# Kernel tuning notes

Hardware: AMD Instinct MI355X
Metric: run time of the kernel (lower is better)

The kernel has to match this reference:

```python
import jax, jax.numpy as jnp
import numpy as np
import math

EMBED_DIM = 1024
N_HEAD = 16
HEAD_DIM = EMBED_DIM // N_HEAD


def setup_inputs() -> dict:
    key = jax.random.key(0)
    ks = jax.random.split(key, 9)
    B, T, C = 4, 2048, EMBED_DIM
    s = 1.0 / math.sqrt(C)
    return {
        "x": jax.random.normal(ks[0], (B, T, C), dtype=jnp.float32),
        "Wq": jax.random.normal(ks[1], (C, C), dtype=jnp.float32) * s,
        "bq": jnp.zeros((C,), dtype=jnp.float32),
        "Wk": jax.random.normal(ks[2], (C, C), dtype=jnp.float32) * s,
        "bk": jnp.zeros((C,), dtype=jnp.float32),
        "Wv": jax.random.normal(ks[3], (C, C), dtype=jnp.float32) * s,
        "bv": jnp.zeros((C,), dtype=jnp.float32),
        "Wp": jax.random.normal(ks[4], (C, C), dtype=jnp.float32) * s,
        "bp": jnp.zeros((C,), dtype=jnp.float32),
    }


def reference(x, Wq, bq, Wk, bk, Wv, bv, Wp, bp):
    B, T, C = x.shape
    H, D = N_HEAD, HEAD_DIM

    def heads(W, b):
        # [B,T,C] -> [B,H,T,D]
        return (x @ W.T + b).reshape(B, T, H, D).transpose(0, 2, 1, 3)

    q = heads(Wq, bq)
    k = heads(Wk, bk)
    v = heads(Wv, bv)

    att = jnp.einsum("bhtd,bhsd->bhts", q, k) * (1.0 / math.sqrt(D))
    causal = jnp.tril(jnp.ones((T, T), dtype=bool))
    att = jnp.where(causal[None, None], att, -jnp.inf)
    att = jax.nn.softmax(att, axis=-1)
    y = jnp.einsum("bhts,bhsd->bhtd", att, v)  # [B,H,T,D]
    y = y.transpose(0, 2, 1, 3).reshape(B, T, C)
    return y @ Wp.T + bp
```

## Files before the change

kernel.cpp:

```cpp
#include <hip/hip_runtime.h>
#include <hip/hip_bf16.h>
#include <cstdint>
#include <cstddef>

#define TQ 2048
#define CDIM 1024
#define NH 16
#define HD 64

typedef __attribute__((ext_vector_type(8))) short bf16x8;
typedef __attribute__((ext_vector_type(4))) float f32x4;
typedef __attribute__((ext_vector_type(16))) float f32x16;

__device__ __forceinline__ unsigned short f2bf(float f) {
  union { float f; unsigned u; } x; x.f = f;
  unsigned r = x.u + 0x7fffu + ((x.u >> 16) & 1u);
  return (unsigned short)(r >> 16);
}

__device__ __forceinline__ unsigned cvtpk(float lo, float hi) {
  unsigned r;
  asm("v_cvt_pk_bf16_f32 %0, %1, %2" : "=v"(r) : "v"(lo), "v"(hi));
  return r;
}

__device__ __forceinline__ void plswap(unsigned& x, unsigned& y) {
  asm("v_permlane32_swap_b32 %0, %1" : "+v"(x), "+v"(y));
}

__device__ __forceinline__ float exp2_fast(float x) {
  float r;
  asm("v_exp_f32 %0, %1" : "=v"(r) : "v"(x));
  return r;
}

__device__ __forceinline__ void gload_lds16(const void* g, void* l) {
  typedef __attribute__((address_space(1))) const void gv;
  typedef __attribute__((address_space(3))) void lv;
  __builtin_amdgcn_global_load_lds((gv*)g, (lv*)l, 16, 0, 0);
}

#define BAR() do { asm volatile("" ::: "memory"); __builtin_amdgcn_s_barrier(); asm volatile("" ::: "memory"); } while (0)
#define VMC2() asm volatile("s_waitcnt vmcnt(2)" ::: "memory")
#define VMC0() asm volatile("s_waitcnt vmcnt(0)" ::: "memory")

__global__ void cvt_all_kernel(const float* __restrict__ x,
                               const float* __restrict__ w0, const float* __restrict__ w1,
                               const float* __restrict__ w2, const float* __restrict__ w3,
                               unsigned short* __restrict__ xb,
                               unsigned short* __restrict__ wb) {
  const int bid = (int)blockIdx.x;
  if (bid < 4096) {
    for (int i = bid * 256 + threadIdx.x; i < 2097152; i += 4096 * 256) {
      float4 v = *(const float4*)(x + (size_t)i * 4);
      ushort4 o;
      o.x = f2bf(v.x); o.y = f2bf(v.y); o.z = f2bf(v.z); o.w = f2bf(v.w);
      *(ushort4*)(xb + (size_t)i * 4) = o;
    }
  } else {
    int i = (bid - 4096) * 256 + threadIdx.x;
    int which = i >> 18;
    const float* src = which == 0 ? w0 : which == 1 ? w1 : which == 2 ? w2 : w3;
    int off = (i & 262143) * 4;
    float4 v = *(const float4*)(src + off);
    ushort4 o;
    o.x = f2bf(v.x); o.y = f2bf(v.y); o.z = f2bf(v.z); o.w = f2bf(v.w);
    *(ushort4*)(wb + (size_t)i * 4) = o;
  }
}

template <int EPI>
__global__ __launch_bounds__(512, 2) void gemm256_kernel(
    const unsigned short* __restrict__ A,
    const unsigned short* __restrict__ Bt,
    const float* __restrict__ b0, const float* __restrict__ b1,
    void* __restrict__ outp,
    int M, int N, int K) {
  __shared__ __align__(16) char lds[131072];

  const int tid = (int)threadIdx.x;
  const int w = tid >> 6, lane = tid & 63;
  const int g = lane >> 4, c = lane & 15;
  const int wm = w >> 2, wn = w & 3;

  const int nbm = M >> 8, nbn = N >> 8;
  const int nwg = nbm * nbn;
  int id = (int)blockIdx.x;
  const int cpx = nwg >> 3;
  id = (id & 7) * cpx + (id >> 3);
  const int tn = id % nbn, tm = id / nbn;

  const char* Ab = (const char*)(A + (size_t)tm * 256 * K);
  const char* Bb = (const char*)(Bt + (size_t)tn * 256 * K);
  const int rowB = K * 2;
  const int nht = (K >> 6) << 2;

  char* aw = lds + wm * 16384;
  char* bw = lds + 65536 + (wn >> 1) * 16384;
  const int bfo = (wn & 1) * 8;

  auto stage_ht = [&](int j) {
    if (j >= nht) return;
    const int t = j >> 2, part = j & 3;
    const int isB = part >> 1, half = part & 1;
    const char* src = isB ? Bb : Ab;
    char* dst = lds + isB * 65536 + (t & 1) * 32768 + half * 16384 + w * 2048;
#pragma unroll
    for (int r = 0; r < 2; ++r) {
      const int f = w * 2 + r;
      const int m16 = f >> 1, ki = f & 1;
      gload_lds16(src + (size_t)(half * 128 + m16 * 16 + c) * rowB +
                      t * 128 + ki * 64 + g * 16,
                  dst + r * 1024);
    }
  };

  f32x4 acc[8][4];
#pragma unroll
  for (int i = 0; i < 8; ++i)
#pragma unroll
    for (int j = 0; j < 4; ++j) acc[i][j] = (f32x4){0.f, 0.f, 0.f, 0.f};
  bf16x8 af[4][2], bv[2][2];

  auto rdA = [&](int buf, int ms) {
#pragma unroll
    for (int mi = 0; mi < 4; ++mi)
#pragma unroll
      for (int ki = 0; ki < 2; ++ki)
        af[mi][ki] = *(const bf16x8*)(aw + buf * 32768 +
                                      ((ms * 4 + mi) * 2 + ki) * 1024 + lane * 16);
  };
  auto rdB = [&](int buf, int ns) {
#pragma unroll
    for (int ni = 0; ni < 2; ++ni)
#pragma unroll
      for (int ki = 0; ki < 2; ++ki)
        bv[ni][ki] = *(const bf16x8*)(bw + buf * 32768 +
                                      (bfo + (ns * 2 + ni) * 2 + ki) * 1024 + lane * 16);
  };
  auto mm = [&](int ms, int ns) {
    __builtin_amdgcn_s_setprio(1);
#pragma unroll
    for (int mi = 0; mi < 4; ++mi)
#pragma unroll
      for (int ni = 0; ni < 2; ++ni)
#pragma unroll
        for (int ki = 0; ki < 2; ++ki)
          acc[ms * 4 + mi][ns * 2 + ni] = __builtin_amdgcn_mfma_f32_16x16x32_bf16(
              af[mi][ki], bv[ni][ki], acc[ms * 4 + mi][ns * 2 + ni], 0, 0, 0);
    __builtin_amdgcn_s_setprio(0);
  };

  for (int j = 0; j < 5; ++j) stage_ht(j);
  VMC2();
  BAR();

  const int niter = K >> 7;
#pragma unroll 1
  for (int i = 0; i < niter; ++i) {
    const int j0 = 5 + (i << 3);
    rdA(0, 0); rdB(0, 0); stage_ht(j0 + 0); BAR(); mm(0, 0); BAR();
    rdB(0, 1);            stage_ht(j0 + 1); BAR(); mm(0, 1); BAR();
    rdA(0, 1);            stage_ht(j0 + 2); BAR(); mm(1, 1); BAR();
    rdB(0, 0);            stage_ht(j0 + 3);
    if (i + 1 < niter) { VMC2(); } else { VMC0(); }
    BAR(); mm(1, 0); BAR();
    rdA(1, 0); rdB(1, 0); stage_ht(j0 + 4); BAR(); mm(0, 0); BAR();
    rdB(1, 1);            stage_ht(j0 + 5); BAR(); mm(0, 1); BAR();
    rdA(1, 1);            stage_ht(j0 + 6); BAR(); mm(1, 1); BAR();
    rdB(1, 0);            stage_ht(j0 + 7); VMC2(); BAR(); mm(1, 0); BAR();
  }

#pragma unroll
  for (int mi = 0; mi < 8; ++mi) {
#pragma unroll
    for (int ni = 0; ni < 4; ++ni) {
      const int n = tn * 256 + wn * 64 + ni * 16 + c;
#pragma unroll
      for (int e = 0; e < 4; ++e) {
        const int m = tm * 256 + wm * 128 + mi * 16 + g * 4 + e;
        float v = acc[mi][ni][e];
        if (EPI == 4) {
          unsigned short* O = (unsigned short*)outp;
          if (n < 1024) {
            v = (v + b0[n]) * 0.18033688f;
            size_t idx = ((size_t)(m >> 11) * NH + (n >> 6)) * (TQ * HD) +
                         (size_t)(m & (TQ - 1)) * HD + (n & (HD - 1));
            O[idx] = f2bf(v);
          } else {
            int nn = n - 1024;
            v += b1[nn];
            size_t idx = 8388608 + ((size_t)(m >> 11) * NH + (nn >> 6)) * (TQ * HD) +
                         (size_t)(m & (TQ - 1)) * HD + (nn & (HD - 1));
            O[idx] = f2bf(v);
          }
        }
      }
    }
  }
}

template <int EPI, int ROWMAJ>
__global__ __launch_bounds__(512, 2) void gemm128x256_kernel(
    const unsigned short* __restrict__ A,
    const unsigned short* __restrict__ Bt,
    const float* __restrict__ b0, const float* __restrict__ b1,
    void* __restrict__ outp,
    int M, int N, int K) {
  __shared__ __align__(16) char lds[98304];

  const int tid = (int)threadIdx.x;
  const int w = tid >> 6, lane = tid & 63;
  const int g = lane >> 4, c = lane & 15;
  const int wm = w >> 2, wn = w & 3;

  const int nbm = M >> 7, nbn = N >> 8;
  const int nwg = nbm * nbn;
  int id = (int)blockIdx.x;
  const int cpx = nwg >> 3;
  id = (id & 7) * cpx + (id >> 3);
  const int tm = ROWMAJ ? (id / nbn) : (id % nbm);
  const int tn = ROWMAJ ? (id % nbn) : (id / nbm);

  const char* Ab = (const char*)(A + (size_t)tm * 128 * K);
  const char* Bb = (const char*)(Bt + (size_t)tn * 256 * K);
  const int rowB = K * 2;
  const int nt = K >> 6;

  auto stageA = [&](int t) {
    if (t >= nt) return;
    char* dst = lds + (t & 1) * 49152 + (w << 11);
    const char* s = Ab + (size_t)(w * 16 + c) * rowB + t * 128 + g * 16;
    gload_lds16(s, dst);
    gload_lds16(s + 64, dst + 1024);
  };
  auto stageB = [&](int t, int odd) {
    if (t >= nt) return;
    const int n16 = (w >> 1) * 4 + 2 * odd + (w & 1);
    char* dst = lds + (t & 1) * 49152 + 16384 + (n16 << 11);
    const char* s = Bb + (size_t)(n16 * 16 + c) * rowB + t * 128 + g * 16;
    gload_lds16(s, dst);
    gload_lds16(s + 64, dst + 1024);
  };

  f32x4 acc[4][4];
#pragma unroll
  for (int i = 0; i < 4; ++i)
#pragma unroll
    for (int j = 0; j < 4; ++j) acc[i][j] = (f32x4){0.f, 0.f, 0.f, 0.f};
  bf16x8 af[2][2], bv[2][2][2];

  auto rdA = [&](int cur, int ms) {
#pragma unroll
    for (int mi2 = 0; mi2 < 2; ++mi2)
#pragma unroll
      for (int ki = 0; ki < 2; ++ki)
        af[mi2][ki] = *(const bf16x8*)(lds + cur * 49152 +
            (((wm * 4 + ms * 2 + mi2) << 1) + ki) * 1024 + lane * 16);
  };
  auto rdB = [&](int cur, int ns) {
#pragma unroll
    for (int ni2 = 0; ni2 < 2; ++ni2)
#pragma unroll
      for (int ki = 0; ki < 2; ++ki)
        bv[ns][ni2][ki] = *(const bf16x8*)(lds + cur * 49152 + 16384 +
            (((wn * 4 + ns * 2 + ni2) << 1) + ki) * 1024 + lane * 16);
  };
  auto mm = [&](int ms, int ns) {
    __builtin_amdgcn_s_setprio(1);
#pragma unroll
    for (int mi2 = 0; mi2 < 2; ++mi2)
#pragma unroll
      for (int ni2 = 0; ni2 < 2; ++ni2)
#pragma unroll
        for (int ki = 0; ki < 2; ++ki)
          acc[ms * 2 + mi2][ns * 2 + ni2] = __builtin_amdgcn_mfma_f32_16x16x32_bf16(
              af[mi2][ki], bv[ns][ni2][ki], acc[ms * 2 + mi2][ns * 2 + ni2], 0, 0, 0);
    __builtin_amdgcn_s_setprio(0);
  };

  stageA(0); stageB(0, 0); stageB(0, 1);
  VMC2();
  BAR();

#pragma unroll 1
  for (int i = 0; i < (nt >> 1); ++i) {
    const int t0 = 2 * i, t1 = 2 * i + 1;
    rdA(0, 0); rdB(0, 0); stageA(t0 + 1);
    mm(0, 0); VMC2(); BAR();
    rdB(0, 1); stageB(t0 + 1, 0);
    mm(0, 1); BAR();
    rdA(0, 1); stageB(t0 + 1, 1);
    mm(1, 1); BAR();
    mm(1, 0); VMC2(); BAR();
    rdA(1, 0); rdB(1, 0); stageA(t1 + 1);
    mm(0, 0);
    if (t1 == nt - 1) { VMC0(); } else { VMC2(); }
    BAR();
    rdB(1, 1); stageB(t1 + 1, 0);
    mm(0, 1); BAR();
    rdA(1, 1); stageB(t1 + 1, 1);
    mm(1, 1); BAR();
    mm(1, 0); VMC2(); BAR();
  }

#pragma unroll
  for (int mi = 0; mi < 4; ++mi) {
#pragma unroll
    for (int ni = 0; ni < 4; ++ni) {
      const int n = tn * 256 + wn * 64 + ni * 16 + c;
#pragma unroll
      for (int e = 0; e < 4; ++e) {
        const int m = tm * 128 + wm * 64 + mi * 16 + g * 4 + e;
        float v = acc[mi][ni][e];
        if (EPI == 1) {
          v += b0[m];
          size_t idx = ((size_t)(n >> 11) * (NH * HD) + m) * TQ + (n & (TQ - 1));
          ((unsigned short*)outp)[idx] = f2bf(v);
        } else if (EPI == 2) {
          v += b0[n];
          ((float*)outp)[(size_t)m * N + n] = v;
        }
      }
    }
  }
}

__global__ __launch_bounds__(256, 4) void attn_kernel(
    const unsigned short* __restrict__ Q,
    const unsigned short* __restrict__ K,
    const unsigned short* __restrict__ Vt,
    unsigned short* __restrict__ Y) {
  __shared__ __align__(16) char Ks[2][8192];
  __shared__ __align__(16) char Vs[2][8192];

  const int tid = (int)threadIdx.x;
  const int w = tid >> 6, lane = tid & 63;
  const int l31 = lane & 31, hi = lane >> 5;

  const int n = (int)blockIdx.x;
  const int g = n & 255, k = n >> 8;
  const int bh = g >> 2;
  const int u = 2 * (g & 3) + (k >> 1);
  const int qt = (k & 1) ? (15 - u) : u;
  const int b = bh >> 4, h = bh & 15;

  const unsigned short* Qb = Q + (size_t)bh * TQ * HD;
  const char* Kb = (const char*)(K + (size_t)bh * TQ * HD);
  const char* Vb = (const char*)(Vt + (size_t)bh * HD * TQ);

  auto stage = [&](int buf, int kt) {
#pragma unroll
    for (int i = 0; i < 2; ++i) {
      const int s = i * 256 + tid;
      const int r32 = (s >> 8) * 32 + (s & 31);
      const int ck = ((s >> 6) & 3) * 32 + ((s >> 5) & 1) * 16;
      char* kdst = &Ks[buf][0] + i * 4096 + (w << 10);
      char* vdst = &Vs[buf][0] + i * 4096 + (w << 10);
      gload_lds16(Kb + (size_t)kt * 8192 + r32 * 128 + ck, kdst);
      gload_lds16(Vb + (size_t)r32 * 4096 + kt * 128 + ck, vdst);
    }
  };

  const int q0 = qt * 128 + w * 32;
  const int qg = q0 + l31;
  const int nkv = 2 * qt + 2;

  stage(0, 0);

  bf16x8 qf[4];
#pragma unroll
  for (int dk = 0; dk < 4; ++dk)
    qf[dk] = *(const bf16x8*)(Qb + (size_t)qg * HD + dk * 16 + hi * 8);

  f32x16 oac[2];
#pragma unroll
  for (int nb = 0; nb < 2; ++nb)
#pragma unroll
    for (int r = 0; r < 16; ++r) oac[nb][r] = 0.f;
  float mr = -3.0e38f, lr = 0.f;

  __syncthreads();

  for (int kt = 0; kt < nkv; ++kt) {
    const int cur = kt & 1;
    if (kt + 1 < nkv) stage(cur ^ 1, kt + 1);

    if (kt * 64 <= q0 + 31) {
      const char* Klane = &Ks[cur][0] + lane * 16;
      const char* Vlane = &Vs[cur][0] + lane * 16;

      f32x16 s0, s1;
#pragma unroll
      for (int r = 0; r < 16; ++r) { s0[r] = 0.f; s1[r] = 0.f; }
#pragma unroll
      for (int dk = 0; dk < 4; ++dk) {
        bf16x8 kf0 = *(const bf16x8*)(Klane + (dk << 10));
        bf16x8 kf1 = *(const bf16x8*)(Klane + ((4 + dk) << 10));
        s0 = __builtin_amdgcn_mfma_f32_32x32x16_bf16(kf0, qf[dk], s0, 0, 0, 0);
        s1 = __builtin_amdgcn_mfma_f32_32x32x16_bf16(kf1, qf[dk], s1, 0, 0, 0);
      }

      const bool maskT = (kt * 64 + 63 > q0);
      if (maskT) {
#pragma unroll
        for (int r = 0; r < 16; ++r) {
          int kv0 = kt * 64 + ((r & 3) + 8 * (r >> 2)) + 4 * hi;
          s0[r] = (kv0 <= qg) ? s0[r] : -3.0e38f;
          s1[r] = (kv0 + 32 <= qg) ? s1[r] : -3.0e38f;
        }
      }

      float mt_ = s0[0];
#pragma unroll
      for (int r = 1; r < 16; ++r) mt_ = fmaxf(mt_, s0[r]);
#pragma unroll
      for (int r = 0; r < 16; ++r) mt_ = fmaxf(mt_, s1[r]);
      mt_ = fmaxf(mt_, __shfl_xor(mt_, 32));

      if (!__all(mt_ - mr <= 8.0f)) {
        const float mn = fmaxf(mr, mt_);
        const float al = exp2_fast(mr - mn);
        mr = mn;
        lr *= al;
#pragma unroll
        for (int nb = 0; nb < 2; ++nb)
#pragma unroll
          for (int r = 0; r < 16; ++r) oac[nb][r] *= al;
      }

      float rs = 0.f;
#pragma unroll
      for (int r = 0; r < 16; ++r) { s0[r] = exp2_fast(s0[r] - mr); rs += s0[r]; }
#pragma unroll
      for (int r = 0; r < 16; ++r) { s1[r] = exp2_fast(s1[r] - mr); rs += s1[r]; }
      rs += __shfl_xor(rs, 32);
      lr += rs;

      bf16x8 pf[4];
      {
        unsigned a0 = cvtpk(s0[0], s0[1]), b0 = cvtpk(s0[2], s0[3]);
        unsigned c0 = cvtpk(s0[4], s0[5]), d0 = cvtpk(s0[6], s0[7]);
        plswap(a0, c0); plswap(b0, d0);
        unsigned a1 = cvtpk(s0[8], s0[9]), b1 = cvtpk(s0[10], s0[11]);
        unsigned c1 = cvtpk(s0[12], s0[13]), d1 = cvtpk(s0[14], s0[15]);
        plswap(a1, c1); plswap(b1, d1);
        unsigned a2 = cvtpk(s1[0], s1[1]), b2 = cvtpk(s1[2], s1[3]);
        unsigned c2 = cvtpk(s1[4], s1[5]), d2 = cvtpk(s1[6], s1[7]);
        plswap(a2, c2); plswap(b2, d2);
        unsigned a3 = cvtpk(s1[8], s1[9]), b3 = cvtpk(s1[10], s1[11]);
        unsigned c3 = cvtpk(s1[12], s1[13]), d3 = cvtpk(s1[14], s1[15]);
        plswap(a3, c3); plswap(b3, d3);
        union { unsigned u[4]; bf16x8 v; } t;
        t.u[0] = a0; t.u[1] = b0; t.u[2] = c0; t.u[3] = d0; pf[0] = t.v;
        t.u[0] = a1; t.u[1] = b1; t.u[2] = c1; t.u[3] = d1; pf[1] = t.v;
        t.u[0] = a2; t.u[1] = b2; t.u[2] = c2; t.u[3] = d2; pf[2] = t.v;
        t.u[0] = a3; t.u[1] = b3; t.u[2] = c3; t.u[3] = d3; pf[3] = t.v;
      }

#pragma unroll
      for (int nb = 0; nb < 2; ++nb)
#pragma unroll
        for (int ks = 0; ks < 4; ++ks) {
          bf16x8 vf = *(const bf16x8*)(Vlane + (((nb << 2) + ks) << 10));
          oac[nb] = __builtin_amdgcn_mfma_f32_32x32x16_bf16(vf, pf[ks], oac[nb], 0, 0, 0);
        }
    }
    __syncthreads();
  }

  float inv;
  asm("v_rcp_f32 %0, %1" : "=v"(inv) : "v"(lr));
  unsigned short* Yrow = Y + (size_t)(b * TQ + qg) * CDIM + h * 64;
#pragma unroll
  for (int nb = 0; nb < 2; ++nb)
#pragma unroll
    for (int j = 0; j < 8; ++j) {
      const int dbase = ((2 * j) & 3) + 8 * (j >> 1);
      unsigned lo = f2bf(oac[nb][2 * j] * inv);
      unsigned hi2 = f2bf(oac[nb][2 * j + 1] * inv);
      *(unsigned*)(Yrow + nb * 32 + dbase + 4 * hi) = lo | (hi2 << 16);
    }
}

extern "C" void kernel_launch(void* const* d_in, const int* in_sizes, int n_in,
                              void* d_out, int out_size, void* d_ws, size_t ws_size,
                              hipStream_t stream) {
  (void)in_sizes; (void)n_in; (void)out_size; (void)ws_size;
  const float* x  = (const float*)d_in[0];
  const float* Wq = (const float*)d_in[1];
  const float* bq = (const float*)d_in[2];
  const float* Wk = (const float*)d_in[3];
  const float* bk = (const float*)d_in[4];
  const float* Wv = (const float*)d_in[5];
  const float* bv = (const float*)d_in[6];
  const float* Wp = (const float*)d_in[7];
  const float* bp = (const float*)d_in[8];
  float* out = (float*)d_out;

  char* ws = (char*)d_ws;
  unsigned short* xb  = (unsigned short*)(ws + 0);
  unsigned short* wqb = (unsigned short*)(ws + 16777216);
  unsigned short* wvb = (unsigned short*)(ws + 20971520);
  unsigned short* wpb = (unsigned short*)(ws + 23068672);
  unsigned short* Qh  = (unsigned short*)(ws + 25165824);
  unsigned short* Kh  = (unsigned short*)(ws + 41943040);
  unsigned short* Vt  = (unsigned short*)(ws + 58720256);
  unsigned short* y   = (unsigned short*)(ws + 75497472);

  cvt_all_kernel<<<8192, 256, 0, stream>>>(x, Wq, Wk, Wv, Wp, xb, wqb);

  gemm256_kernel<4><<<256, 512, 0, stream>>>(xb, wqb, bq, bk, Qh, 8192, 2048, 1024);
  gemm128x256_kernel<1, 0><<<256, 512, 0, stream>>>(wvb, xb, bv, bv, Vt, 1024, 8192, 1024);

  attn_kernel<<<1024, 256, 0, stream>>>(Qh, Kh, Vt, y);

  gemm128x256_kernel<2, 1><<<256, 512, 0, stream>>>(y, wpb, bp, bp, out, 8192, 1024, 1024);
}
```

Measured before the change: 196.8 us.

## Process two heads per attention block to raise per-wave ILP

Each attention workgroup now handles the same query tile for two (batch, head) pairs, staging K/V for both into a 64KB double-buffered LDS region and interleaving their independent QK, softmax and PV chains. The grid is halved to 512 blocks and launch bounds drop to 2 blocks per CU. The intent is to expose more independent MFMA and exp work per wave to hide latency. The cost is higher register and LDS use, which lowers occupancy, and fewer blocks to balance the causal work.

```diff
diff --git a/kernel.cpp b/kernel.cpp
--- a/kernel.cpp
+++ b/kernel.cpp
@@ -326,28 +326,31 @@
   }
 }
 
-__global__ __launch_bounds__(256, 4) void attn_kernel(
+__global__ __launch_bounds__(256, 2) void attn_kernel(
     const unsigned short* __restrict__ Q,
     const unsigned short* __restrict__ K,
     const unsigned short* __restrict__ Vt,
     unsigned short* __restrict__ Y) {
-  __shared__ __align__(16) char Ks[2][8192];
-  __shared__ __align__(16) char Vs[2][8192];
+  __shared__ __align__(16) char L[2][32768];
 
   const int tid = (int)threadIdx.x;
   const int w = tid >> 6, lane = tid & 63;
   const int l31 = lane & 31, hi = lane >> 5;
 
-  const int n = (int)blockIdx.x;
-  const int g = n & 255, k = n >> 8;
-  const int bh = g >> 2;
-  const int u = 2 * (g & 3) + (k >> 1);
-  const int qt = (k & 1) ? (15 - u) : u;
-  const int b = bh >> 4, h = bh & 15;
-
-  const unsigned short* Qb = Q + (size_t)bh * TQ * HD;
-  const char* Kb = (const char*)(K + (size_t)bh * TQ * HD);
-  const char* Vb = (const char*)(Vt + (size_t)bh * HD * TQ);
+  const int z = (int)blockIdx.x;
+  const int kk = z >> 8, r_ = z & 255;
+  const int u = r_ & 7, bhp = r_ >> 3;
+  const int qt = kk ? (15 - u) : u;
+  const int bh0 = 2 * bhp, bh1 = 2 * bhp + 1;
+  const int b0i = bh0 >> 4, h0 = bh0 & 15;
+  const int b1i = bh1 >> 4, h1 = bh1 & 15;
+
+  const unsigned short* QbA = Q + (size_t)bh0 * TQ * HD;
+  const unsigned short* QbB = Q + (size_t)bh1 * TQ * HD;
+  const char* KbA = (const char*)(K + (size_t)bh0 * TQ * HD);
+  const char* KbB = (const char*)(K + (size_t)bh1 * TQ * HD);
+  const char* VbA = (const char*)(Vt + (size_t)bh0 * HD * TQ);
+  const char* VbB = (const char*)(Vt + (size_t)bh1 * HD * TQ);
 
   auto stage = [&](int buf, int kt) {
 #pragma unroll
@@ -355,10 +358,12 @@
       const int s = i * 256 + tid;
       const int r32 = (s >> 8) * 32 + (s & 31);
       const int ck = ((s >> 6) & 3) * 32 + ((s >> 5) & 1) * 16;
-      char* kdst = &Ks[buf][0] + i * 4096 + (w << 10);
-      char* vdst = &Vs[buf][0] + i * 4096 + (w << 10);
-      gload_lds16(Kb + (size_t)kt * 8192 + r32 * 128 + ck, kdst);
-      gload_lds16(Vb + (size_t)r32 * 4096 + kt * 128 + ck, vdst);
+      const int doff = i * 4096 + (w << 10);
+      char* base = &L[buf][0];
+      gload_lds16(KbA + (size_t)kt * 8192 + r32 * 128 + ck, base + doff);
+      gload_lds16(KbB + (size_t)kt * 8192 + r32 * 128 + ck, base + 8192 + doff);
+      gload_lds16(VbA + (size_t)r32 * 4096 + kt * 128 + ck, base + 16384 + doff);
+      gload_lds16(VbB + (size_t)r32 * 4096 + kt * 128 + ck, base + 24576 + doff);
     }
   };
 
@@ -368,17 +373,19 @@
 
   stage(0, 0);
 
-  bf16x8 qf[4];
-#pragma unroll
-  for (int dk = 0; dk < 4; ++dk)
-    qf[dk] = *(const bf16x8*)(Qb + (size_t)qg * HD + dk * 16 + hi * 8);
-
-  f32x16 oac[2];
+  bf16x8 qfA[4], qfB[4];
+#pragma unroll
+  for (int dk = 0; dk < 4; ++dk) {
+    qfA[dk] = *(const bf16x8*)(QbA + (size_t)qg * HD + dk * 16 + hi * 8);
+    qfB[dk] = *(const bf16x8*)(QbB + (size_t)qg * HD + dk * 16 + hi * 8);
+  }
+
+  f32x16 oacA[2], oacB[2];
 #pragma unroll
   for (int nb = 0; nb < 2; ++nb)
 #pragma unroll
-    for (int r = 0; r < 16; ++r) oac[nb][r] = 0.f;
-  float mr = -3.0e38f, lr = 0.f;
+    for (int r = 0; r < 16; ++r) { oacA[nb][r] = 0.f; oacB[nb][r] = 0.f; }
+  float mrA = -3.0e38f, lrA = 0.f, mrB = -3.0e38f, lrB = 0.f;
 
   __syncthreads();
 
@@ -387,18 +394,27 @@
     if (kt + 1 < nkv) stage(cur ^ 1, kt + 1);
 
     if (kt * 64 <= q0 + 31) {
-      const char* Klane = &Ks[cur][0] + lane * 16;
-      const char* Vlane = &Vs[cur][0] + lane * 16;
-
-      f32x16 s0, s1;
-#pragma unroll
-      for (int r = 0; r < 16; ++r) { s0[r] = 0.f; s1[r] = 0.f; }
+      const char* KlA = &L[cur][0] + lane * 16;
+      const char* KlB = KlA + 8192;
+      const char* VlA = KlA + 16384;
+      const char* VlB = KlA + 24576;
+
+      f32x16 sA0, sA1, sB0, sB1;
+#pragma unroll
+      for (int r = 0; r < 16; ++r) { sA0[r] = 0.f; sA1[r] = 0.f; sB0[r] = 0.f; sB1[r] = 0.f; }
 #pragma unroll
       for (int dk = 0; dk < 4; ++dk) {
-        bf16x8 kf0 = *(const bf16x8*)(Klane + (dk << 10));
-        bf16x8 kf1 = *(const bf16x8*)(Klane + ((4 + dk) << 10));
-        s0 = __builtin_amdgcn_mfma_f32_32x32x16_bf16(kf0, qf[dk], s0, 0, 0, 0);
-        s1 = __builtin_amdgcn_mfma_f32_32x32x16_bf16(kf1, qf[dk], s1, 0, 0, 0);
+        bf16x8 kf0 = *(const bf16x8*)(KlA + (dk << 10));
+        bf16x8 kf1 = *(const bf16x8*)(KlA + ((4 + dk) << 10));
+        sA0 = __builtin_amdgcn_mfma_f32_32x32x16_bf16(kf0, qfA[dk], sA0, 0, 0, 0);
+        sA1 = __builtin_amdgcn_mfma_f32_32x32x16_bf16(kf1, qfA[dk], sA1, 0, 0, 0);
+      }
+#pragma unroll
+      for (int dk = 0; dk < 4; ++dk) {
+        bf16x8 kf0 = *(const bf16x8*)(KlB + (dk << 10));
+        bf16x8 kf1 = *(const bf16x8*)(KlB + ((4 + dk) << 10));
+        sB0 = __builtin_amdgcn_mfma_f32_32x32x16_bf16(kf0, qfB[dk], sB0, 0, 0, 0);
+        sB1 = __builtin_amdgcn_mfma_f32_32x32x16_bf16(kf1, qfB[dk], sB1, 0, 0, 0);
       }
 
       const bool maskT = (kt * 64 + 63 > q0);
@@ -406,80 +422,141 @@
 #pragma unroll
         for (int r = 0; r < 16; ++r) {
           int kv0 = kt * 64 + ((r & 3) + 8 * (r >> 2)) + 4 * hi;
-          s0[r] = (kv0 <= qg) ? s0[r] : -3.0e38f;
-          s1[r] = (kv0 + 32 <= qg) ? s1[r] : -3.0e38f;
-        }
-      }
-
-      float mt_ = s0[0];
-#pragma unroll
-      for (int r = 1; r < 16; ++r) mt_ = fmaxf(mt_, s0[r]);
-#pragma unroll
-      for (int r = 0; r < 16; ++r) mt_ = fmaxf(mt_, s1[r]);
-      mt_ = fmaxf(mt_, __shfl_xor(mt_, 32));
-
-      if (!__all(mt_ - mr <= 8.0f)) {
-        const float mn = fmaxf(mr, mt_);
-        const float al = exp2_fast(mr - mn);
-        mr = mn;
-        lr *= al;
+          bool ok0 = (kv0 <= qg), ok1 = (kv0 + 32 <= qg);
+          sA0[r] = ok0 ? sA0[r] : -3.0e38f;
+          sA1[r] = ok1 ? sA1[r] : -3.0e38f;
+          sB0[r] = ok0 ? sB0[r] : -3.0e38f;
+          sB1[r] = ok1 ? sB1[r] : -3.0e38f;
+        }
+      }
+
+      {
+        float mt_ = sA0[0];
+#pragma unroll
+        for (int r = 1; r < 16; ++r) mt_ = fmaxf(mt_, sA0[r]);
+#pragma unroll
+        for (int r = 0; r < 16; ++r) mt_ = fmaxf(mt_, sA1[r]);
+        mt_ = fmaxf(mt_, __shfl_xor(mt_, 32));
+        if (!__all(mt_ - mrA <= 8.0f)) {
+          const float mn = fmaxf(mrA, mt_);
+          const float al = exp2_fast(mrA - mn);
+          mrA = mn;
+          lrA *= al;
+#pragma unroll
+          for (int nb = 0; nb < 2; ++nb)
+#pragma unroll
+            for (int r = 0; r < 16; ++r) oacA[nb][r] *= al;
+        }
+        float rs = 0.f;
+#pragma unroll
+        for (int r = 0; r < 16; ++r) { sA0[r] = exp2_fast(sA0[r] - mrA); rs += sA0[r]; }
+#pragma unroll
+        for (int r = 0; r < 16; ++r) { sA1[r] = exp2_fast(sA1[r] - mrA); rs += sA1[r]; }
+        rs += __shfl_xor(rs, 32);
+        lrA += rs;
+
+        bf16x8 pf[4];
+        {
+          unsigned a0 = cvtpk(sA0[0], sA0[1]), b0 = cvtpk(sA0[2], sA0[3]);
+          unsigned c0 = cvtpk(sA0[4], sA0[5]), d0 = cvtpk(sA0[6], sA0[7]);
+          plswap(a0, c0); plswap(b0, d0);
+          unsigned a1 = cvtpk(sA0[8], sA0[9]), b1 = cvtpk(sA0[10], sA0[11]);
+          unsigned c1 = cvtpk(sA0[12], sA0[13]), d1 = cvtpk(sA0[14], sA0[15]);
+          plswap(a1, c1); plswap(b1, d1);
+          unsigned a2 = cvtpk(sA1[0], sA1[1]), b2 = cvtpk(sA1[2], sA1[3]);
+          unsigned c2 = cvtpk(sA1[4], sA1[5]), d2 = cvtpk(sA1[6], sA1[7]);
+          plswap(a2, c2); plswap(b2, d2);
+          unsigned a3 = cvtpk(sA1[8], sA1[9]), b3 = cvtpk(sA1[10], sA1[11]);
+          unsigned c3 = cvtpk(sA1[12], sA1[13]), d3 = cvtpk(sA1[14], sA1[15]);
+          plswap(a3, c3); plswap(b3, d3);
+          union { unsigned u[4]; bf16x8 v; } t;
+          t.u[0] = a0; t.u[1] = b0; t.u[2] = c0; t.u[3] = d0; pf[0] = t.v;
+          t.u[0] = a1; t.u[1] = b1; t.u[2] = c1; t.u[3] = d1; pf[1] = t.v;
+          t.u[0] = a2; t.u[1] = b2; t.u[2] = c2; t.u[3] = d2; pf[2] = t.v;
+          t.u[0] = a3; t.u[1] = b3; t.u[2] = c3; t.u[3] = d3; pf[3] = t.v;
+        }
 #pragma unroll
         for (int nb = 0; nb < 2; ++nb)
 #pragma unroll
-          for (int r = 0; r < 16; ++r) oac[nb][r] *= al;
-      }
-
-      float rs = 0.f;
-#pragma unroll
-      for (int r = 0; r < 16; ++r) { s0[r] = exp2_fast(s0[r] - mr); rs += s0[r]; }
-#pragma unroll
-      for (int r = 0; r < 16; ++r) { s1[r] = exp2_fast(s1[r] - mr); rs += s1[r]; }
-      rs += __shfl_xor(rs, 32);
-      lr += rs;
-
-      bf16x8 pf[4];
+          for (int ks = 0; ks < 4; ++ks) {
+            bf16x8 vf = *(const bf16x8*)(VlA + (((nb << 2) + ks) << 10));
+            oacA[nb] = __builtin_amdgcn_mfma_f32_32x32x16_bf16(vf, pf[ks], oacA[nb], 0, 0, 0);
+          }
+      }
+
       {
-        unsigned a0 = cvtpk(s0[0], s0[1]), b0 = cvtpk(s0[2], s0[3]);
-        unsigned c0 = cvtpk(s0[4], s0[5]), d0 = cvtpk(s0[6], s0[7]);
-        plswap(a0, c0); plswap(b0, d0);
-        unsigned a1 = cvtpk(s0[8], s0[9]), b1 = cvtpk(s0[10], s0[11]);
-        unsigned c1 = cvtpk(s0[12], s0[13]), d1 = cvtpk(s0[14], s0[15]);
-        plswap(a1, c1); plswap(b1, d1);
-        unsigned a2 = cvtpk(s1[0], s1[1]), b2 = cvtpk(s1[2], s1[3]);
-        unsigned c2 = cvtpk(s1[4], s1[5]), d2 = cvtpk(s1[6], s1[7]);
-        plswap(a2, c2); plswap(b2, d2);
-        unsigned a3 = cvtpk(s1[8], s1[9]), b3 = cvtpk(s1[10], s1[11]);
-        unsigned c3 = cvtpk(s1[12], s1[13]), d3 = cvtpk(s1[14], s1[15]);
-        plswap(a3, c3); plswap(b3, d3);
-        union { unsigned u[4]; bf16x8 v; } t;
-        t.u[0] = a0; t.u[1] = b0; t.u[2] = c0; t.u[3] = d0; pf[0] = t.v;
-        t.u[0] = a1; t.u[1] = b1; t.u[2] = c1; t.u[3] = d1; pf[1] = t.v;
-        t.u[0] = a2; t.u[1] = b2; t.u[2] = c2; t.u[3] = d2; pf[2] = t.v;
-        t.u[0] = a3; t.u[1] = b3; t.u[2] = c3; t.u[3] = d3; pf[3] = t.v;
-      }
-
-#pragma unroll
-      for (int nb = 0; nb < 2; ++nb)
-#pragma unroll
-        for (int ks = 0; ks < 4; ++ks) {
-          bf16x8 vf = *(const bf16x8*)(Vlane + (((nb << 2) + ks) << 10));
-          oac[nb] = __builtin_amdgcn_mfma_f32_32x32x16_bf16(vf, pf[ks], oac[nb], 0, 0, 0);
-        }
+        float mt_ = sB0[0];
+#pragma unroll
+        for (int r = 1; r < 16; ++r) mt_ = fmaxf(mt_, sB0[r]);
+#pragma unroll
+        for (int r = 0; r < 16; ++r) mt_ = fmaxf(mt_, sB1[r]);
+        mt_ = fmaxf(mt_, __shfl_xor(mt_, 32));
+        if (!__all(mt_ - mrB <= 8.0f)) {
+          const float mn = fmaxf(mrB, mt_);
+          const float al = exp2_fast(mrB - mn);
+          mrB = mn;
+          lrB *= al;
+#pragma unroll
+          for (int nb = 0; nb < 2; ++nb)
+#pragma unroll
+            for (int r = 0; r < 16; ++r) oacB[nb][r] *= al;
+        }
+        float rs = 0.f;
+#pragma unroll
+        for (int r = 0; r < 16; ++r) { sB0[r] = exp2_fast(sB0[r] - mrB); rs += sB0[r]; }
+#pragma unroll
+        for (int r = 0; r < 16; ++r) { sB1[r] = exp2_fast(sB1[r] - mrB); rs += sB1[r]; }
+        rs += __shfl_xor(rs, 32);
+        lrB += rs;
+
+        bf16x8 pf[4];
+        {
+          unsigned a0 = cvtpk(sB0[0], sB0[1]), b0 = cvtpk(sB0[2], sB0[3]);
+          unsigned c0 = cvtpk(sB0[4], sB0[5]), d0 = cvtpk(sB0[6], sB0[7]);
+          plswap(a0, c0); plswap(b0, d0);
+          unsigned a1 = cvtpk(sB0[8], sB0[9]), b1 = cvtpk(sB0[10], sB0[11]);
+          unsigned c1 = cvtpk(sB0[12], sB0[13]), d1 = cvtpk(sB0[14], sB0[15]);
+          plswap(a1, c1); plswap(b1, d1);
+          unsigned a2 = cvtpk(sB1[0], sB1[1]), b2 = cvtpk(sB1[2], sB1[3]);
+          unsigned c2 = cvtpk(sB1[4], sB1[5]), d2 = cvtpk(sB1[6], sB1[7]);
+          plswap(a2, c2); plswap(b2, d2);
+          unsigned a3 = cvtpk(sB1[8], sB1[9]), b3 = cvtpk(sB1[10], sB1[11]);
+          unsigned c3 = cvtpk(sB1[12], sB1[13]), d3 = cvtpk(sB1[14], sB1[15]);
+          plswap(a3, c3); plswap(b3, d3);
+          union { unsigned u[4]; bf16x8 v; } t;
+          t.u[0] = a0; t.u[1] = b0; t.u[2] = c0; t.u[3] = d0; pf[0] = t.v;
+          t.u[0] = a1; t.u[1] = b1; t.u[2] = c1; t.u[3] = d1; pf[1] = t.v;
+          t.u[0] = a2; t.u[1] = b2; t.u[2] = c2; t.u[3] = d2; pf[2] = t.v;
+          t.u[0] = a3; t.u[1] = b3; t.u[2] = c3; t.u[3] = d3; pf[3] = t.v;
+        }
+#pragma unroll
+        for (int nb = 0; nb < 2; ++nb)
+#pragma unroll
+          for (int ks = 0; ks < 4; ++ks) {
+            bf16x8 vf = *(const bf16x8*)(VlB + (((nb << 2) + ks) << 10));
+            oacB[nb] = __builtin_amdgcn_mfma_f32_32x32x16_bf16(vf, pf[ks], oacB[nb], 0, 0, 0);
+          }
+      }
     }
     __syncthreads();
   }
 
-  float inv;
-  asm("v_rcp_f32 %0, %1" : "=v"(inv) : "v"(lr));
-  unsigned short* Yrow = Y + (size_t)(b * TQ + qg) * CDIM + h * 64;
+  float invA, invB;
+  asm("v_rcp_f32 %0, %1" : "=v"(invA) : "v"(lrA));
+  asm("v_rcp_f32 %0, %1" : "=v"(invB) : "v"(lrB));
+  unsigned short* YrowA = Y + (size_t)(b0i * TQ + qg) * CDIM + h0 * 64;
+  unsigned short* YrowB = Y + (size_t)(b1i * TQ + qg) * CDIM + h1 * 64;
 #pragma unroll
   for (int nb = 0; nb < 2; ++nb)
 #pragma unroll
     for (int j = 0; j < 8; ++j) {
       const int dbase = ((2 * j) & 3) + 8 * (j >> 1);
-      unsigned lo = f2bf(oac[nb][2 * j] * inv);
-      unsigned hi2 = f2bf(oac[nb][2 * j + 1] * inv);
-      *(unsigned*)(Yrow + nb * 32 + dbase + 4 * hi) = lo | (hi2 << 16);
+      unsigned loA = f2bf(oacA[nb][2 * j] * invA);
+      unsigned hiA = f2bf(oacA[nb][2 * j + 1] * invA);
+      *(unsigned*)(YrowA + nb * 32 + dbase + 4 * hi) = loA | (hiA << 16);
+      unsigned loB = f2bf(oacB[nb][2 * j] * invB);
+      unsigned hiB = f2bf(oacB[nb][2 * j + 1] * invB);
+      *(unsigned*)(YrowB + nb * 32 + dbase + 4 * hi) = loB | (hiB << 16);
     }
 }
 
@@ -513,7 +590,7 @@
   gemm256_kernel<4><<<256, 512, 0, stream>>>(xb, wqb, bq, bk, Qh, 8192, 2048, 1024);
   gemm128x256_kernel<1, 0><<<256, 512, 0, stream>>>(wvb, xb, bv, bv, Vt, 1024, 8192, 1024);
 
-  attn_kernel<<<1024, 256, 0, stream>>>(Qh, Kh, Vt, y);
+  attn_kernel<<<512, 256, 0, stream>>>(Qh, Kh, Vt, y);
 
   gemm128x256_kernel<2, 1><<<256, 512, 0, stream>>>(y, wpb, bp, bp, out, 8192, 1024, 1024);
 }
```

After: 201.5 us. 1.02x slower.
